# Optimization experiments

Measured on AMD Instinct MI355X. Metric: run time of the kernel, lower is better.

Reference implementation:

```python
import jax, jax.numpy as jnp
import numpy as np


def conv2d(x, w, b, pad):
    out = jax.lax.conv_general_dilated(x, w, (1, 1), ((pad, pad), (pad, pad)),
                                       dimension_numbers=('NCHW', 'OIHW', 'NCHW'))
    return out + b[None, :, None, None]


def silu(x):
    return x * jax.nn.sigmoid(x)


def group_norm(x, g, b, groups, eps=1e-5):
    B, C, H, W = x.shape
    xg = x.reshape(B, groups, C // groups, H, W)
    m = xg.mean(axis=(2, 3, 4), keepdims=True)
    v = xg.var(axis=(2, 3, 4), keepdims=True)
    xg = (xg - m) * jax.lax.rsqrt(v + eps)
    return xg.reshape(B, C, H, W) * g[None, :, None, None] + b[None, :, None, None]


def snake_cumsum(off):
    # off: [B,K,H,W]. Center kernel point has zero offset; points accumulate
    # outward from center (the 'snake' bend), as in DSCNet.
    K = off.shape[1]
    c = K // 2
    upper = jnp.cumsum(off[:, c + 1:], axis=1)
    lower = jnp.flip(jnp.cumsum(jnp.flip(off[:, :c], axis=1), axis=1), axis=1)
    return jnp.concatenate([lower, jnp.zeros_like(off[:, :1]), upper], axis=1)


def bilinear_gather(img, ys, xs):
    # img [B,C,H,W]; ys,xs [B,K,H,W] float coords -> sampled [B,C,K,H,W]
    B, C, H, W = img.shape
    K = ys.shape[1]
    ys = jnp.clip(ys, 0.0, H - 1.0)
    xs = jnp.clip(xs, 0.0, W - 1.0)
    y0f = jnp.floor(ys)
    x0f = jnp.floor(xs)
    wy = (ys - y0f)[:, None]  # [B,1,K,H,W]
    wx = (xs - x0f)[:, None]
    y0 = y0f.astype(jnp.int32)
    x0 = x0f.astype(jnp.int32)
    y1 = jnp.minimum(y0 + 1, H - 1)
    x1 = jnp.minimum(x0 + 1, W - 1)
    flat = img.reshape(B, C, H * W)

    def gat(yi, xi):
        idx = (yi * W + xi).reshape(B, -1)  # [B, K*H*W]
        g = jnp.take_along_axis(flat, idx[:, None, :], axis=2)
        return g.reshape(B, C, K, H, W)

    return (gat(y0, x0) * (1 - wy) * (1 - wx) + gat(y0, x1) * (1 - wy) * wx
            + gat(y1, x0) * wy * (1 - wx) + gat(y1, x1) * wy * wx)


def dsconv(x, off_w, off_b, dsc_w, dsc_b, gn_g, gn_b, morph, extend_scope=1.0):
    # Dynamic snake conv for one morphology.
    # morph 0: kernel spreads along x, bends in y; morph 1: opposite.
    B, C, H, W = x.shape
    K = dsc_w.shape[-1]
    c = K // 2
    off = jnp.tanh(conv2d(x, off_w, off_b, pad=1))  # [B,2K,H,W]; BN folded into conv bias
    bend = snake_cumsum(off[:, :K] if morph == 0 else off[:, K:])  # [B,K,H,W]
    spread = (jnp.arange(K) - c).astype(x.dtype)[None, :, None, None]
    hh = jnp.arange(H, dtype=x.dtype)[None, None, :, None]
    ww = jnp.arange(W, dtype=x.dtype)[None, None, None, :]
    if morph == 0:
        ys = hh + extend_scope * bend
        xs = jnp.broadcast_to(ww + spread, ys.shape)
    else:
        xs = ww + extend_scope * bend
        ys = jnp.broadcast_to(hh + spread, xs.shape)
    sampled = bilinear_gather(x, ys, xs)  # [B,C,K,H,W]
    # k-point conv over the stacked snake axis == (K,1)/(1,K) conv with stride K
    out = jnp.einsum('bckhw,ock->bohw', sampled, dsc_w) + dsc_b[None, :, None, None]
    O = dsc_w.shape[0]
    return jax.nn.relu(group_norm(out, gn_g, gn_b, groups=O // 4))


def dysnake_conv(x, p):
    # DySnakeConv: standard conv + snake-x + snake-y, concat, 1x1 fuse
    kpad = p['conv0_w'].shape[-1] // 2
    a = silu(conv2d(x, p['conv0_w'], p['conv0_b'], pad=kpad))
    bx = dsconv(x, p['offx_w'], p['offx_b'], p['dscx_w'], p['dscx_b'], p['gnx_g'], p['gnx_b'], morph=0)
    by = dsconv(x, p['offy_w'], p['offy_b'], p['dscy_w'], p['dscy_b'], p['gny_g'], p['gny_b'], morph=1)
    cat = jnp.concatenate([a, bx, by], axis=1)  # [B,3*ouc,H,W]
    return silu(jnp.einsum('bchw,oc->bohw', cat, p['fuse_w']) + p['fuse_b'][None, :, None, None])


_PNAMES = ['conv0_w', 'conv0_b', 'offx_w', 'offx_b', 'dscx_w', 'dscx_b', 'gnx_g', 'gnx_b',
           'offy_w', 'offy_b', 'dscy_w', 'dscy_b', 'gny_g', 'gny_b', 'fuse_w', 'fuse_b']


def setup_inputs() -> dict:
    key = jax.random.key(0)
    ks = iter(jax.random.split(key, 64))

    def rn(shape, s=0.05):
        return jax.random.normal(next(ks), shape, dtype=jnp.float32) * s

    B, H, W = 8, 80, 80
    c1, c2, c_ = 256, 256, 128
    kk = 3

    def block(inc, ouc, pre):
        return {
            pre + 'conv0_w': rn((ouc, inc, kk, kk)), pre + 'conv0_b': rn((ouc,)),
            pre + 'offx_w': rn((2 * kk, inc, 3, 3)), pre + 'offx_b': rn((2 * kk,)),
            pre + 'dscx_w': rn((ouc, inc, kk)), pre + 'dscx_b': rn((ouc,)),
            pre + 'gnx_g': jnp.ones((ouc,), jnp.float32), pre + 'gnx_b': jnp.zeros((ouc,), jnp.float32),
            pre + 'offy_w': rn((2 * kk, inc, 3, 3)), pre + 'offy_b': rn((2 * kk,)),
            pre + 'dscy_w': rn((ouc, inc, kk)), pre + 'dscy_b': rn((ouc,)),
            pre + 'gny_g': jnp.ones((ouc,), jnp.float32), pre + 'gny_b': jnp.zeros((ouc,), jnp.float32),
            pre + 'fuse_w': rn((ouc, 3 * ouc)), pre + 'fuse_b': rn((ouc,)),
        }

    inp = {'x': jax.random.normal(next(ks), (B, c1, H, W), dtype=jnp.float32)}
    inp.update(block(c1, c_, 'cv1_'))
    inp.update(block(c_, c2, 'cv2_'))
    return inp


def reference(x, cv1_conv0_w, cv1_conv0_b, cv1_offx_w, cv1_offx_b, cv1_dscx_w, cv1_dscx_b,
              cv1_gnx_g, cv1_gnx_b, cv1_offy_w, cv1_offy_b, cv1_dscy_w, cv1_dscy_b,
              cv1_gny_g, cv1_gny_b, cv1_fuse_w, cv1_fuse_b,
              cv2_conv0_w, cv2_conv0_b, cv2_offx_w, cv2_offx_b, cv2_dscx_w, cv2_dscx_b,
              cv2_gnx_g, cv2_gnx_b, cv2_offy_w, cv2_offy_b, cv2_dscy_w, cv2_dscy_b,
              cv2_gny_g, cv2_gny_b, cv2_fuse_w, cv2_fuse_b):
    p1 = dict(zip(_PNAMES, (cv1_conv0_w, cv1_conv0_b, cv1_offx_w, cv1_offx_b, cv1_dscx_w, cv1_dscx_b,
                            cv1_gnx_g, cv1_gnx_b, cv1_offy_w, cv1_offy_b, cv1_dscy_w, cv1_dscy_b,
                            cv1_gny_g, cv1_gny_b, cv1_fuse_w, cv1_fuse_b)))
    p2 = dict(zip(_PNAMES, (cv2_conv0_w, cv2_conv0_b, cv2_offx_w, cv2_offx_b, cv2_dscx_w, cv2_dscx_b,
                            cv2_gnx_g, cv2_gnx_b, cv2_offy_w, cv2_offy_b, cv2_dscy_w, cv2_dscy_b,
                            cv2_gny_g, cv2_gny_b, cv2_fuse_w, cv2_fuse_b)))
    h = dysnake_conv(x, p1)
    h = dysnake_conv(h, p2)
    return x + h  # shortcut and c1 == c2
```

## Files before the change

### kernel.cpp

```cpp
#include <hip/hip_runtime.h>
#include <cstddef>

#define B_   8
#define H_   80
#define W_   80
#define HW   6400
#define W2   82
#define HW2  6724

typedef __attribute__((ext_vector_type(8)))  short short8;
typedef __attribute__((ext_vector_type(16))) float f32x16;

__device__ __forceinline__ float bf2f(ushort u) {
    return __uint_as_float(((unsigned)u) << 16);
}
__device__ __forceinline__ ushort f2bf(float f) {
    unsigned u = __float_as_uint(f);
    u += 0x7FFF + ((u >> 16) & 1);
    return (ushort)(u >> 16);
}
__device__ __forceinline__ f32x16 mfma16(short8 a, short8 b, f32x16 c) {
    return __builtin_amdgcn_mfma_f32_32x32x16_bf16(a, b, c, 0, 0, 0);
}
__device__ __forceinline__ void async16(const void* g, void* l) {
    __builtin_amdgcn_global_load_lds(
        (const __attribute__((address_space(1))) unsigned int*)g,
        (__attribute__((address_space(3))) unsigned int*)l, 16, 0, 0);
}
__device__ __forceinline__ const ushort* frag_ptr(const ushort* sbuf, int row, int c8l) {
    return sbuf + row * 64 + ((c8l ^ (row & 7)) << 3);
}

__global__ __launch_bounds__(256) void halo_zero2_kernel(
    ushort* __restrict__ xp1, ushort* __restrict__ xp2) {
    int idx = blockIdx.x * 256 + threadIdx.x;
    const int n1 = B_ * 324 * 32;
    const int n2 = B_ * 324 * 16;
    ushort* xp; int C, slots, i;
    if (idx < n1) { xp = xp1; C = 256; slots = 32; i = idx; }
    else if (idx < n1 + n2) { xp = xp2; C = 128; slots = 16; i = idx - n1; }
    else return;
    int sl = i % slots;
    int t = i / slots;
    int p = t % 324;
    int b = t / 324;
    int h, w;
    if (p < 164) { h = (p < 82) ? 0 : 81; w = p % 82; }
    else { int q = p - 164; w = (q < 80) ? 0 : 81; h = 1 + (q % 80); }
    *(uint4*)(xp + ((size_t)(b * HW2 + h * W2 + w)) * C + sl * 8) =
        make_uint4(0, 0, 0, 0);
}

__global__ __launch_bounds__(256) void transpose_x_kernel(
    const float* __restrict__ x, ushort* __restrict__ xp, int C) {
    __shared__ float s[64][65];
    int hw0 = blockIdx.x * 64, c0 = blockIdx.y * 64, b = blockIdx.z;
    int t = threadIdx.x;
    int hl = t & 63, cq = t >> 6;
    #pragma unroll
    for (int i = 0; i < 16; i++) {
        int cl = cq * 16 + i;
        s[cl][hl] = x[((size_t)(b * C + c0 + cl)) * HW + hw0 + hl];
    }
    __syncthreads();
    int cl = t & 63, hq = t >> 6;
    #pragma unroll
    for (int i = 0; i < 16; i++) {
        int hl2 = hq * 16 + i;
        int hw = hw0 + hl2;
        int h = hw / W_, w = hw - h * W_;
        xp[((size_t)(b * HW2 + (h + 1) * W2 + w + 1)) * C + c0 + cl] = f2bf(s[cl][hl2]);
    }
}

__global__ __launch_bounds__(256) void final_add_kernel(
    const float* __restrict__ x, const ushort* __restrict__ h2,
    float* __restrict__ out, int C) {
    __shared__ float s[64][65];
    int hw0 = blockIdx.x * 64, c0 = blockIdx.y * 64, b = blockIdx.z;
    int t = threadIdx.x;
    int cl = t & 63, hq = t >> 6;
    #pragma unroll
    for (int i = 0; i < 16; i++) {
        int hl = hq * 16 + i;
        s[cl][hl] = bf2f(h2[((size_t)(b * HW + hw0 + hl)) * C + c0 + cl]);
    }
    __syncthreads();
    int hl = t & 63, cq = t >> 6;
    #pragma unroll
    for (int i = 0; i < 16; i++) {
        int cl2 = cq * 16 + i;
        size_t o = ((size_t)(b * C + c0 + cl2)) * HW + hw0 + hl;
        out[o] = x[o] + s[cl2][hl];
    }
}

struct WJobs {
    const float* src[8];
    ushort* dst[8];
    int cin[8], t[8];
    int start[9];
};

__global__ __launch_bounds__(256) void wprep_all_kernel(WJobs J) {
    int idx = blockIdx.x * 256 + threadIdx.x;
    if (idx >= J.start[8]) return;
    int j = 0;
    #pragma unroll
    for (int k = 1; k < 8; k++) if (idx >= J.start[k]) j = k;
    int i = idx - J.start[j];
    int CIN = J.cin[j], T = J.t[j];
    int oc = i / (CIN * T);
    int r = i - oc * CIN * T;
    int ci = r / T, t_ = r - ci * T;
    J.dst[j][((size_t)oc * T + t_) * CIN + ci] = f2bf(J.src[j][i]);
}

__global__ void wprep_off_kernel(const float* __restrict__ wx_,
                                 const float* __restrict__ bx_,
                                 const float* __restrict__ wy_,
                                 const float* __restrict__ by_,
                                 ushort* __restrict__ dst,
                                 float* __restrict__ bdst, int CIN) {
    int idx = blockIdx.x * 256 + threadIdx.x;
    if (idx < 4) {
        const int chs[4] = {0, 2, 3, 5};
        bdst[idx] = (idx < 2) ? bx_[chs[idx]] : by_[chs[idx]];
    }
    if (idx >= 32 * 9 * CIN) return;
    int oc = idx / (9 * CIN);
    int r = idx - oc * 9 * CIN;
    int tap = r / CIN, ci = r - tap * CIN;
    float v = 0.f;
    if (oc < 4) {
        const int chs[4] = {0, 2, 3, 5};
        const float* src = (oc < 2) ? wx_ : wy_;
        v = src[((size_t)chs[oc] * CIN + ci) * 9 + tap];
    }
    dst[idx] = f2bf(v);
}

__global__ __launch_bounds__(256, 2) void off_conv_mfma_kernel(
    const ushort* __restrict__ xp, const ushort* __restrict__ wB,
    const float* __restrict__ bias, float* __restrict__ off4, int CIN) {
    __shared__ ushort s_x[162 * 64];
    __shared__ ushort s_w[144 * 64];
    int tid = threadIdx.x;
    int ty0 = (blockIdx.x / 5) * 16, tx0 = (blockIdx.x % 5) * 16;
    int b = blockIdx.y;
    int lane = tid & 63, wid = tid >> 6;
    int l31 = lane & 31, kg = lane >> 5;
    int pym[2], pxm[2];
    #pragma unroll
    for (int mf = 0; mf < 2; mf++) {
        int p = wid * 64 + mf * 32 + l31;
        pym[mf] = p >> 4; pxm[mf] = p & 15;
    }
    f32x16 acc[2] = {};
    for (int c0 = 0; c0 < CIN; c0 += 32) {
        __syncthreads();
        for (int u = tid; u < 1296; u += 256) {
            int pid = u >> 2, ci8 = u & 3;
            int r = pid / 18, c = pid - r * 18;
            int py = ty0 + r, px = tx0 + c;
            uint4 v = *(const uint4*)(xp + ((size_t)(b * HW2 + py * W2 + px)) * CIN
                                      + c0 + ci8 * 8);
            int row = pid >> 1;
            int phys = (((pid & 1) << 2) + ci8) ^ (row & 7);
            *(uint4*)(s_x + row * 64 + phys * 8) = v;
        }
        for (int cc = wid; cc < 18; cc += 4) {
            int L = cc * 64 + lane;
            int row = L >> 3, phys = L & 7;
            int logical = phys ^ (row & 7);
            int tap = row >> 4, ocp = row & 15;
            int oc = ocp * 2 + (logical >> 2), ci8 = logical & 3;
            async16(wB + ((size_t)oc * 9 + tap) * CIN + c0 + ci8 * 8,
                    s_w + (size_t)L * 8);
        }
        __syncthreads();
        #pragma unroll
        for (int tap = 0; tap < 9; tap++) {
            int dy = tap / 3, dx = tap - dy * 3;
            int wrow = tap * 16 + (l31 >> 1);
            #pragma unroll
            for (int ks = 0; ks < 2; ks++) {
                int blk = ks * 2 + kg;
                int wphys = (((l31 & 1) << 2) + blk) ^ (wrow & 7);
                short8 bfr = *(const short8*)(s_w + wrow * 64 + wphys * 8);
                #pragma unroll
                for (int mf = 0; mf < 2; mf++) {
                    int pix = (pym[mf] + dy) * 18 + (pxm[mf] + dx);
                    int xrow = pix >> 1;
                    int xphys = (((pix & 1) << 2) + blk) ^ (xrow & 7);
                    short8 afr = *(const short8*)(s_x + xrow * 64 + xphys * 8);
                    acc[mf] = mfma16(afr, bfr, acc[mf]);
                }
            }
        }
    }
    int oc = l31;
    if (oc < 4) {
        float bb = bias[oc];
        #pragma unroll
        for (int mf = 0; mf < 2; mf++) {
            #pragma unroll
            for (int reg = 0; reg < 16; reg++) {
                int row = (reg & 3) + 8 * (reg >> 2) + 4 * kg;
                int p = wid * 64 + mf * 32 + row;
                int y = ty0 + (p >> 4), x = tx0 + (p & 15);
                off4[((size_t)b * 4 + oc) * HW + y * W_ + x] = tanhf(acc[mf][reg] + bb);
            }
        }
    }
}

__global__ __launch_bounds__(256, 4) void convdsc_kernel(
    const ushort* __restrict__ xp,
    const ushort* __restrict__ wC, const float* __restrict__ biasC,
    ushort* __restrict__ outC,
    const float* __restrict__ off4,
    const ushort* __restrict__ Bwx, const float* __restrict__ biasx,
    ushort* __restrict__ outx,
    const ushort* __restrict__ Bwy, const float* __restrict__ biasy,
    ushort* __restrict__ outy, float* __restrict__ stat, int CIN, int OC) {
    __shared__ ushort s_a[128 * 64];
    __shared__ ushort s_b[128 * 64];
    __shared__ int   s_i0[3][128];
    __shared__ int   s_i1[3][128];
    __shared__ float s_wl[3][128];
    int tid = threadIdx.x;
    int m0 = blockIdx.x * 128, n0 = blockIdx.y * 128;
    int b = m0 / HW, hw0 = m0 - b * HW;
    int lane = tid & 63, wid = tid >> 6;
    int l31 = lane & 31, kg = lane >> 5;
    int wm = wid >> 1, wn = wid & 1;

    if (blockIdx.z == 0) {
        const ushort* xpb = xp + (size_t)b * HW2 * CIN;
        const ushort* asrc[4];
        #pragma unroll
        for (int j = 0; j < 4; j++) {
            int s = (wid * 4 + j) * 64 + lane;
            int r = s >> 3, c8p = s & 7;
            int c8l = c8p ^ (r & 7);
            int hw = hw0 + r;
            int h = hw / W_, w = hw - h * W_;
            asrc[j] = xpb + ((size_t)((h + 1) * W2 + (w + 1))) * CIN + c8l * 8;
        }
        f32x16 acc[2][2] = {};
        int K = 9 * CIN, nk = K >> 6;
        int tap = 0, cioff = 0;
        for (int kc = 0; kc < nk; kc++) {
            int kg64 = kc << 6;
            int dy = tap / 3, dx = tap - dy * 3;
            int soff = ((dy - 1) * W2 + (dx - 1)) * CIN + cioff;
            __syncthreads();
            #pragma unroll
            for (int j = 0; j < 4; j++) {
                int s = (wid * 4 + j) * 64 + lane;
                int r = s >> 3, c8p = s & 7;
                int c8l = c8p ^ (r & 7);
                async16(wC + (size_t)(n0 + r) * K + kg64 + c8l * 8, s_b + s * 8);
                async16(asrc[j] + soff, s_a + s * 8);
            }
            __syncthreads();
            #pragma unroll
            for (int ks = 0; ks < 4; ks++) {
                int c8l = ks * 2 + kg;
                short8 af0 = *(const short8*)frag_ptr(s_a, wm * 64 + l31, c8l);
                short8 af1 = *(const short8*)frag_ptr(s_a, wm * 64 + 32 + l31, c8l);
                short8 bf0 = *(const short8*)frag_ptr(s_b, wn * 64 + l31, c8l);
                short8 bf1 = *(const short8*)frag_ptr(s_b, wn * 64 + 32 + l31, c8l);
                acc[0][0] = mfma16(af0, bf0, acc[0][0]);
                acc[0][1] = mfma16(af0, bf1, acc[0][1]);
                acc[1][0] = mfma16(af1, bf0, acc[1][0]);
                acc[1][1] = mfma16(af1, bf1, acc[1][1]);
            }
            cioff += 64;
            if (cioff == CIN) { cioff = 0; tap++; }
        }
        #pragma unroll
        for (int nf = 0; nf < 2; nf++) {
            int n = n0 + wn * 64 + nf * 32 + l31;
            float bb = biasC[n];
            #pragma unroll
            for (int mf = 0; mf < 2; mf++) {
                #pragma unroll
                for (int reg = 0; reg < 16; reg++) {
                    int row = (reg & 3) + 8 * (reg >> 2) + 4 * kg;
                    int m = m0 + wm * 64 + mf * 32 + row;
                    float v = acc[mf][nf][reg] + bb;
                    v = v / (1.f + expf(-v));
                    outC[(size_t)m * OC + n] = f2bf(v);
                }
            }
        }
        return;
    }

    int morph = blockIdx.z - 1;
    const ushort* Bw = morph ? Bwy : Bwx;
    const float* bias = morph ? biasy : biasx;
    ushort* out = morph ? outy : outx;
    float* statm = stat + (size_t)morph * B_ * 256 * 2;
    for (int u = tid; u < 384; u += 256) {
        int k3 = u >> 7, r = u & 127;
        int hw = hw0 + r;
        int h = hw / W_, w = hw - h * W_;
        float bend = 0.f;
        if (k3 != 1) {
            int mp = (morph ? 2 : 0) + (k3 >> 1);
            bend = off4[((size_t)b * 4 + mp) * HW + hw];
        }
        int i0, i1; float wl;
        if (morph == 0) {
            float ys = fminf(fmaxf((float)h + bend, 0.f), 79.f);
            float y0f = floorf(ys); wl = ys - y0f;
            int y0 = (int)y0f, y1 = min(y0 + 1, 79);
            int xk = min(max(w + k3 - 1, 0), 79);
            i0 = (y0 + 1) * W2 + xk + 1; i1 = (y1 + 1) * W2 + xk + 1;
        } else {
            float xs = fminf(fmaxf((float)w + bend, 0.f), 79.f);
            float x0f = floorf(xs); wl = xs - x0f;
            int x0 = (int)x0f, x1 = min(x0 + 1, 79);
            int yk = min(max(h + k3 - 1, 0), 79);
            i0 = (yk + 1) * W2 + x0 + 1; i1 = (yk + 1) * W2 + x1 + 1;
        }
        s_i0[k3][r] = i0; s_i1[k3][r] = i1; s_wl[k3][r] = wl;
    }
    const ushort* xb = xp + (size_t)b * HW2 * CIN;
    const ushort* asrcC[4];
    #pragma unroll
    for (int j = 0; j < 4; j++) {
        int s = (wid * 4 + j) * 64 + lane;
        int r = s >> 3, c8p = s & 7;
        int c8l = c8p ^ (r & 7);
        int hw = hw0 + r;
        int h = hw / W_, w = hw - h * W_;
        asrcC[j] = xb + ((size_t)((h + 1) * W2 + (w + 1))) * CIN + c8l * 8;
    }
    f32x16 acc[2][2] = {};
    int K = 3 * CIN, nk = K >> 6;
    for (int kc = 0; kc < nk; kc++) {
        int kg64 = kc << 6;
        int k3 = kg64 / CIN;
        int cioff = kg64 - k3 * CIN;
        __syncthreads();
        #pragma unroll
        for (int j = 0; j < 4; j++) {
            int s = (wid * 4 + j) * 64 + lane;
            int r = s >> 3, c8p = s & 7;
            int c8l = c8p ^ (r & 7);
            async16(Bw + (size_t)(n0 + r) * K + kg64 + c8l * 8, s_b + s * 8);
        }
        if (k3 == 1) {
            #pragma unroll
            for (int j = 0; j < 4; j++) {
                int s = (wid * 4 + j) * 64 + lane;
                async16(asrcC[j] + cioff, s_a + s * 8);
            }
        } else {
            #pragma unroll
            for (int i = 0; i < 4; i++) {
                int s = i * 256 + tid;
                int r = s >> 3, c8p = s & 7;
                int c8l = c8p ^ (r & 7);
                int ci = cioff + c8l * 8;
                float wl = s_wl[k3][r];
                uint4 u0 = *(const uint4*)(xb + (size_t)s_i0[k3][r] * CIN + ci);
                uint4 u1 = *(const uint4*)(xb + (size_t)s_i1[k3][r] * CIN + ci);
                const ushort* p0 = (const ushort*)&u0;
                const ushort* p1 = (const ushort*)&u1;
                uint ov[4];
                #pragma unroll
                for (int j = 0; j < 4; j++) {
                    float a0 = bf2f(p0[2 * j]),     b0 = bf2f(p1[2 * j]);
                    float a1 = bf2f(p0[2 * j + 1]), b1 = bf2f(p1[2 * j + 1]);
                    float r0 = a0 + (b0 - a0) * wl;
                    float r1 = a1 + (b1 - a1) * wl;
                    asm("v_cvt_pk_bf16_f32 %0, %1, %2"
                        : "=v"(ov[j]) : "v"(r0), "v"(r1));
                }
                *(uint4*)(s_a + s * 8) = *(uint4*)ov;
            }
        }
        __syncthreads();
        #pragma unroll
        for (int ks = 0; ks < 4; ks++) {
            int c8l = ks * 2 + kg;
            short8 af0 = *(const short8*)frag_ptr(s_a, wm * 64 + l31, c8l);
            short8 af1 = *(const short8*)frag_ptr(s_a, wm * 64 + 32 + l31, c8l);
            short8 bf0 = *(const short8*)frag_ptr(s_b, wn * 64 + l31, c8l);
            short8 bf1 = *(const short8*)frag_ptr(s_b, wn * 64 + 32 + l31, c8l);
            acc[0][0] = mfma16(af0, bf0, acc[0][0]);
            acc[0][1] = mfma16(af0, bf1, acc[0][1]);
            acc[1][0] = mfma16(af1, bf0, acc[1][0]);
            acc[1][1] = mfma16(af1, bf1, acc[1][1]);
        }
    }
    #pragma unroll
    for (int nf = 0; nf < 2; nf++) {
        int n = n0 + wn * 64 + nf * 32 + l31;
        float bb = bias[n];
        float ssum = 0.f, ssq = 0.f;
        #pragma unroll
        for (int mf = 0; mf < 2; mf++) {
            #pragma unroll
            for (int reg = 0; reg < 16; reg++) {
                int row = (reg & 3) + 8 * (reg >> 2) + 4 * kg;
                int m = m0 + wm * 64 + mf * 32 + row;
                float v = acc[mf][nf][reg] + bb;
                ssum += v; ssq += v * v;
                out[(size_t)m * OC + n] = f2bf(v);
            }
        }
        ssum += __shfl_xor(ssum, 32);
        ssq  += __shfl_xor(ssq, 32);
        if (kg == 0) {
            float* st = statm + ((size_t)b * OC + n) * 2;
            atomicAdd(st, ssum);
            atomicAdd(st + 1, ssq);
        }
    }
}

__global__ __launch_bounds__(256, 4) void gemm128_kernel(
    const ushort* __restrict__ a0, const ushort* __restrict__ a1,
    const ushort* __restrict__ a2, int part_k,
    const ushort* __restrict__ Bw, int K, int N,
    const float* __restrict__ bias,
    const float* __restrict__ scx, const float* __restrict__ shx,
    const float* __restrict__ scy, const float* __restrict__ shy,
    ushort* __restrict__ out, int epi_silu, int out_pad) {
    __shared__ ushort s_a[128 * 64];
    __shared__ ushort s_b[128 * 64];
    int tid = threadIdx.x;
    int m0 = blockIdx.x * 128, n0 = blockIdx.y * 128;
    int b = m0 / HW;
    int lane = tid & 63, wid = tid >> 6;
    int l31 = lane & 31, kg = lane >> 5;
    int wm = wid >> 1, wn = wid & 1;
    f32x16 acc[2][2] = {};
    int nk = K >> 6;
    for (int kc = 0; kc < nk; kc++) {
        int kg64 = kc << 6;
        int part = kg64 / part_k;
        int koff = kg64 - part * part_k;
        __syncthreads();
        #pragma unroll
        for (int j = 0; j < 4; j++) {
            int s = (wid * 4 + j) * 64 + lane;
            int r = s >> 3, c8p = s & 7;
            int c8l = c8p ^ (r & 7);
            async16(Bw + (size_t)(n0 + r) * K + kg64 + c8l * 8, s_b + s * 8);
        }
        if (part == 0) {
            #pragma unroll
            for (int j = 0; j < 4; j++) {
                int s = (wid * 4 + j) * 64 + lane;
                int r = s >> 3, c8p = s & 7;
                int c8l = c8p ^ (r & 7);
                async16(a0 + (size_t)(m0 + r) * part_k + koff + c8l * 8,
                        s_a + s * 8);
            }
        } else {
            const ushort* ap = (part == 1) ? a1 : a2;
            const float* scp = ((part == 1) ? scx : scy) + (size_t)b * part_k;
            const float* shp = ((part == 1) ? shx : shy) + (size_t)b * part_k;
            #pragma unroll
            for (int i = 0; i < 4; i++) {
                int s = i * 256 + tid;
                int r = s >> 3, c8p = s & 7;
                int c8l = c8p ^ (r & 7);
                int ch = koff + c8l * 8;
                uint4 u = *(const uint4*)(ap + (size_t)(m0 + r) * part_k + ch);
                float4 c0 = *(const float4*)(scp + ch);
                float4 c1 = *(const float4*)(scp + ch + 4);
                float4 h0 = *(const float4*)(shp + ch);
                float4 h1 = *(const float4*)(shp + ch + 4);
                const ushort* pv = (const ushort*)&u;
                uint ov[4];
                float r0, r1;
                r0 = fmaxf(bf2f(pv[0]) * c0.x + h0.x, 0.f);
                r1 = fmaxf(bf2f(pv[1]) * c0.y + h0.y, 0.f);
                asm("v_cvt_pk_bf16_f32 %0, %1, %2" : "=v"(ov[0]) : "v"(r0), "v"(r1));
                r0 = fmaxf(bf2f(pv[2]) * c0.z + h0.z, 0.f);
                r1 = fmaxf(bf2f(pv[3]) * c0.w + h0.w, 0.f);
                asm("v_cvt_pk_bf16_f32 %0, %1, %2" : "=v"(ov[1]) : "v"(r0), "v"(r1));
                r0 = fmaxf(bf2f(pv[4]) * c1.x + h1.x, 0.f);
                r1 = fmaxf(bf2f(pv[5]) * c1.y + h1.y, 0.f);
                asm("v_cvt_pk_bf16_f32 %0, %1, %2" : "=v"(ov[2]) : "v"(r0), "v"(r1));
                r0 = fmaxf(bf2f(pv[6]) * c1.z + h1.z, 0.f);
                r1 = fmaxf(bf2f(pv[7]) * c1.w + h1.w, 0.f);
                asm("v_cvt_pk_bf16_f32 %0, %1, %2" : "=v"(ov[3]) : "v"(r0), "v"(r1));
                *(uint4*)(s_a + s * 8) = *(uint4*)ov;
            }
        }
        __syncthreads();
        #pragma unroll
        for (int ks = 0; ks < 4; ks++) {
            int c8l = ks * 2 + kg;
            short8 af0 = *(const short8*)frag_ptr(s_a, wm * 64 + l31, c8l);
            short8 af1 = *(const short8*)frag_ptr(s_a, wm * 64 + 32 + l31, c8l);
            short8 bf0 = *(const short8*)frag_ptr(s_b, wn * 64 + l31, c8l);
            short8 bf1 = *(const short8*)frag_ptr(s_b, wn * 64 + 32 + l31, c8l);
            acc[0][0] = mfma16(af0, bf0, acc[0][0]);
            acc[0][1] = mfma16(af0, bf1, acc[0][1]);
            acc[1][0] = mfma16(af1, bf0, acc[1][0]);
            acc[1][1] = mfma16(af1, bf1, acc[1][1]);
        }
    }
    #pragma unroll
    for (int nf = 0; nf < 2; nf++) {
        int n = n0 + wn * 64 + nf * 32 + l31;
        float bb = bias[n];
        #pragma unroll
        for (int mf = 0; mf < 2; mf++) {
            #pragma unroll
            for (int reg = 0; reg < 16; reg++) {
                int row = (reg & 3) + 8 * (reg >> 2) + 4 * kg;
                int m = m0 + wm * 64 + mf * 32 + row;
                float v = acc[mf][nf][reg] + bb;
                if (epi_silu) v = v / (1.f + expf(-v));
                size_t mm = (size_t)m;
                if (out_pad) {
                    int bb_ = m / HW, hw = m - bb_ * HW;
                    int h = hw / W_, w = hw - h * W_;
                    mm = (size_t)bb_ * HW2 + (h + 1) * W2 + w + 1;
                }
                out[mm * N + n] = f2bf(v);
            }
        }
    }
}

__global__ void gn_finalize_kernel(const float* __restrict__ stat,
                                   const float* __restrict__ gx,
                                   const float* __restrict__ bx,
                                   const float* __restrict__ gy,
                                   const float* __restrict__ by,
                                   float* __restrict__ scx, float* __restrict__ shx,
                                   float* __restrict__ scy, float* __restrict__ shy,
                                   int C) {
    int idx = blockIdx.x * 256 + threadIdx.x;
    if (idx >= B_ * C) return;
    int which = blockIdx.y;
    const float* gamma = which ? gy : gx;
    const float* beta  = which ? by : bx;
    float* sc = which ? scy : scx;
    float* sh = which ? shy : shx;
    int b = idx / C, c = idx - b * C;
    const float* st = stat + (size_t)which * B_ * 256 * 2
                    + ((size_t)b * C + (c & ~3)) * 2;
    float s  = st[0] + st[2] + st[4] + st[6];
    float sq = st[1] + st[3] + st[5] + st[7];
    float mean = s / (4.f * HW);
    float var = sq / (4.f * HW) - mean * mean;
    float rs = rsqrtf(var + 1e-5f);
    float scale = rs * gamma[c];
    sc[idx] = scale;
    sh[idx] = beta[c] - mean * scale;
}

struct BlkBuf {
    ushort *xp, *abuf, *bqx, *bqy, *hout;
    float *off4, *stat, *scx, *shx, *scy, *shy, *boff;
    ushort *wc, *wdx, *wdy, *wf, *woff;
};

static void run_block(const BlkBuf& B, int CIN, int OC,
                      const float* const* P, int out_pad, hipStream_t stream) {
    dim3 blk(256);
    hipMemsetAsync(B.stat, 0, (size_t)2 * B_ * 256 * 2 * 4, stream);
    off_conv_mfma_kernel<<<dim3(25, B_), blk, 0, stream>>>(
        B.xp, B.woff, B.boff, B.off4, CIN);
    convdsc_kernel<<<dim3(400, OC / 128, 3), blk, 0, stream>>>(
        B.xp, B.wc, P[1], B.abuf,
        B.off4, B.wdx, P[5], B.bqx, B.wdy, P[11], B.bqy, B.stat, CIN, OC);
    int fgrid = (B_ * OC + 255) / 256;
    gn_finalize_kernel<<<dim3(fgrid, 2), blk, 0, stream>>>(
        B.stat, P[6], P[7], P[12], P[13], B.scx, B.shx, B.scy, B.shy, OC);
    gemm128_kernel<<<dim3(400, OC / 128), blk, 0, stream>>>(
        B.abuf, B.bqx, B.bqy, OC, B.wf, 3 * OC, OC, P[15],
        B.scx, B.shx, B.scy, B.shy, B.hout, 1, out_pad);
}

extern "C" void kernel_launch(void* const* d_in, const int* in_sizes, int n_in,
                              void* d_out, int out_size, void* d_ws, size_t ws_size,
                              hipStream_t stream) {
    const float* x = (const float*)d_in[0];
    const float* P1[16];
    const float* P2[16];
    for (int i = 0; i < 16; i++) {
        P1[i] = (const float*)d_in[1 + i];
        P2[i] = (const float*)d_in[17 + i];
    }
    char* base = (char*)d_ws;
    size_t off = 0;
    auto alloc = [&](size_t bytes) -> char* {
        off = (off + 255) & ~(size_t)255;
        char* p = base + off;
        off += bytes;
        return p;
    };
    ushort* xp1  = (ushort*)alloc((size_t)B_ * HW2 * 256 * 2);
    ushort* xp2  = (ushort*)alloc((size_t)B_ * HW2 * 128 * 2);
    ushort* abuf = (ushort*)alloc((size_t)B_ * HW * 256 * 2);
    ushort* bqx  = (ushort*)alloc((size_t)B_ * HW * 256 * 2);
    ushort* bqy  = (ushort*)alloc((size_t)B_ * HW * 256 * 2);
    float*  off4 = (float*)alloc((size_t)B_ * 4 * HW * 4);
    float*  stat = (float*)alloc((size_t)2 * B_ * 256 * 2 * 4);
    float*  scx  = (float*)alloc(B_ * 256 * 4);
    float*  shx  = (float*)alloc(B_ * 256 * 4);
    float*  scy  = (float*)alloc(B_ * 256 * 4);
    float*  shy  = (float*)alloc(B_ * 256 * 4);
    ushort* wc1  = (ushort*)alloc((size_t)128 * 9 * 256 * 2);
    ushort* wc2  = (ushort*)alloc((size_t)256 * 9 * 128 * 2);
    ushort* wdx1 = (ushort*)alloc((size_t)128 * 3 * 256 * 2);
    ushort* wdy1 = (ushort*)alloc((size_t)128 * 3 * 256 * 2);
    ushort* wdx2 = (ushort*)alloc((size_t)256 * 3 * 128 * 2);
    ushort* wdy2 = (ushort*)alloc((size_t)256 * 3 * 128 * 2);
    ushort* wf1  = (ushort*)alloc((size_t)128 * 384 * 2);
    ushort* wf2  = (ushort*)alloc((size_t)256 * 768 * 2);
    ushort* wo1  = (ushort*)alloc((size_t)32 * 9 * 256 * 2);
    ushort* wo2  = (ushort*)alloc((size_t)32 * 9 * 128 * 2);
    float*  bo1  = (float*)alloc(32 * 4);
    float*  bo2  = (float*)alloc(32 * 4);
    ushort* h2 = xp1;

    dim3 blk(256);
    {
        int total = B_ * 324 * 32 + B_ * 324 * 16;
        halo_zero2_kernel<<<(total + 255) / 256, blk, 0, stream>>>(xp1, xp2);
    }

    {
        WJobs J;
        const float* srcs[8] = {P1[0], P1[4], P1[10], P1[14],
                                P2[0], P2[4], P2[10], P2[14]};
        ushort* dsts[8] = {wc1, wdx1, wdy1, wf1, wc2, wdx2, wdy2, wf2};
        int cins[8] = {256, 256, 256, 384, 128, 128, 128, 768};
        int ts[8]   = {9, 3, 3, 1, 9, 3, 3, 1};
        int ocs[8]  = {128, 128, 128, 128, 256, 256, 256, 256};
        int acc = 0;
        for (int j = 0; j < 8; j++) {
            J.src[j] = srcs[j]; J.dst[j] = dsts[j];
            J.cin[j] = cins[j]; J.t[j] = ts[j];
            J.start[j] = acc;
            acc += ocs[j] * cins[j] * ts[j];
        }
        J.start[8] = acc;
        wprep_all_kernel<<<(acc + 255) / 256, blk, 0, stream>>>(J);
    }
    wprep_off_kernel<<<(32 * 9 * 256 + 255) / 256, blk, 0, stream>>>(
        P1[2], P1[3], P1[8], P1[9], wo1, bo1, 256);
    wprep_off_kernel<<<(32 * 9 * 128 + 255) / 256, blk, 0, stream>>>(
        P2[2], P2[3], P2[8], P2[9], wo2, bo2, 128);

    transpose_x_kernel<<<dim3(100, 4, B_), blk, 0, stream>>>(x, xp1, 256);

    BlkBuf B1 = {xp1, abuf, bqx, bqy, xp2, off4, stat, scx, shx, scy, shy,
                 bo1, wc1, wdx1, wdy1, wf1, wo1};
    run_block(B1, 256, 128, P1, 1, stream);

    BlkBuf B2 = {xp2, abuf, bqx, bqy, h2, off4, stat, scx, shx, scy, shy,
                 bo2, wc2, wdx2, wdy2, wf2, wo2};
    run_block(B2, 128, 256, P2, 0, stream);

    final_add_kernel<<<dim3(100, 4, B_), blk, 0, stream>>>(x, h2, (float*)d_out, 256);
}
```

Before: 524.7 us.

## Recast offset conv as implicit GEMM with more blocks; restructure GEMM epilogues

The offset convolution kernel moves from 16x16 spatial tiles with a halo (200 blocks, 32-channel chunks) to an implicit-GEMM layout. Each block now takes 128 pixels and walks K in 64-wide chunks using async loads, giving 400 blocks at higher occupancy. The goal is to fill the GPU better for this small-N conv, at the price of losing the halo reuse, so input rows are reloaded once per tap. The epilogues of the three GEMM kernels are also reordered to handle both N fragments in one loop, with the bias loads hoisted and the paired stores interleaved.

```diff
diff --git a/kernel.cpp b/kernel.cpp
--- a/kernel.cpp
+++ b/kernel.cpp
@@ -140,77 +140,63 @@
     dst[idx] = f2bf(v);
 }
 
-__global__ __launch_bounds__(256, 2) void off_conv_mfma_kernel(
+__global__ __launch_bounds__(256, 4) void off_gemm_kernel(
     const ushort* __restrict__ xp, const ushort* __restrict__ wB,
     const float* __restrict__ bias, float* __restrict__ off4, int CIN) {
-    __shared__ ushort s_x[162 * 64];
-    __shared__ ushort s_w[144 * 64];
+    __shared__ ushort s_a[128 * 64];
+    __shared__ ushort s_bo[32 * 64];
     int tid = threadIdx.x;
-    int ty0 = (blockIdx.x / 5) * 16, tx0 = (blockIdx.x % 5) * 16;
-    int b = blockIdx.y;
+    int m0 = blockIdx.x * 128;
+    int b = m0 / HW, hw0 = m0 - b * HW;
     int lane = tid & 63, wid = tid >> 6;
     int l31 = lane & 31, kg = lane >> 5;
-    int pym[2], pxm[2];
-    #pragma unroll
-    for (int mf = 0; mf < 2; mf++) {
-        int p = wid * 64 + mf * 32 + l31;
-        pym[mf] = p >> 4; pxm[mf] = p & 15;
-    }
-    f32x16 acc[2] = {};
-    for (int c0 = 0; c0 < CIN; c0 += 32) {
+    const ushort* xpb = xp + (size_t)b * HW2 * CIN;
+    const ushort* asrc[4];
+    #pragma unroll
+    for (int j = 0; j < 4; j++) {
+        int s = (wid * 4 + j) * 64 + lane;
+        int r = s >> 3, c8p = s & 7;
+        int c8l = c8p ^ (r & 7);
+        int hw = hw0 + r;
+        int h = hw / W_, w = hw - h * W_;
+        asrc[j] = xpb + ((size_t)((h + 1) * W2 + (w + 1))) * CIN + c8l * 8;
+    }
+    int rB = tid >> 3;
+    int cB = (tid & 7) ^ (rB & 7);
+    f32x16 acc = {};
+    int K = 9 * CIN, nk = K >> 6;
+    int tap = 0, cioff = 0;
+    for (int kc = 0; kc < nk; kc++) {
+        int kg64 = kc << 6;
+        int dy = tap / 3, dx = tap - dy * 3;
+        int soff = ((dy - 1) * W2 + (dx - 1)) * CIN + cioff;
         __syncthreads();
-        for (int u = tid; u < 1296; u += 256) {
-            int pid = u >> 2, ci8 = u & 3;
-            int r = pid / 18, c = pid - r * 18;
-            int py = ty0 + r, px = tx0 + c;
-            uint4 v = *(const uint4*)(xp + ((size_t)(b * HW2 + py * W2 + px)) * CIN
-                                      + c0 + ci8 * 8);
-            int row = pid >> 1;
-            int phys = (((pid & 1) << 2) + ci8) ^ (row & 7);
-            *(uint4*)(s_x + row * 64 + phys * 8) = v;
-        }
-        for (int cc = wid; cc < 18; cc += 4) {
-            int L = cc * 64 + lane;
-            int row = L >> 3, phys = L & 7;
-            int logical = phys ^ (row & 7);
-            int tap = row >> 4, ocp = row & 15;
-            int oc = ocp * 2 + (logical >> 2), ci8 = logical & 3;
-            async16(wB + ((size_t)oc * 9 + tap) * CIN + c0 + ci8 * 8,
-                    s_w + (size_t)L * 8);
+        async16(wB + (size_t)rB * K + kg64 + cB * 8, s_bo + (size_t)tid * 8);
+        #pragma unroll
+        for (int j = 0; j < 4; j++) {
+            int s = (wid * 4 + j) * 64 + lane;
+            async16(asrc[j] + soff, s_a + s * 8);
         }
         __syncthreads();
         #pragma unroll
-        for (int tap = 0; tap < 9; tap++) {
-            int dy = tap / 3, dx = tap - dy * 3;
-            int wrow = tap * 16 + (l31 >> 1);
-            #pragma unroll
-            for (int ks = 0; ks < 2; ks++) {
-                int blk = ks * 2 + kg;
-                int wphys = (((l31 & 1) << 2) + blk) ^ (wrow & 7);
-                short8 bfr = *(const short8*)(s_w + wrow * 64 + wphys * 8);
-                #pragma unroll
-                for (int mf = 0; mf < 2; mf++) {
-                    int pix = (pym[mf] + dy) * 18 + (pxm[mf] + dx);
-                    int xrow = pix >> 1;
-                    int xphys = (((pix & 1) << 2) + blk) ^ (xrow & 7);
-                    short8 afr = *(const short8*)(s_x + xrow * 64 + xphys * 8);
-                    acc[mf] = mfma16(afr, bfr, acc[mf]);
-                }
-            }
-        }
+        for (int ks = 0; ks < 4; ks++) {
+            int c8l = ks * 2 + kg;
+            short8 af = *(const short8*)frag_ptr(s_a, wid * 32 + l31, c8l);
+            short8 bf = *(const short8*)frag_ptr(s_bo, l31, c8l);
+            acc = mfma16(af, bf, acc);
+        }
+        cioff += 64;
+        if (cioff == CIN) { cioff = 0; tap++; }
     }
     int oc = l31;
     if (oc < 4) {
         float bb = bias[oc];
         #pragma unroll
-        for (int mf = 0; mf < 2; mf++) {
-            #pragma unroll
-            for (int reg = 0; reg < 16; reg++) {
-                int row = (reg & 3) + 8 * (reg >> 2) + 4 * kg;
-                int p = wid * 64 + mf * 32 + row;
-                int y = ty0 + (p >> 4), x = tx0 + (p & 15);
-                off4[((size_t)b * 4 + oc) * HW + y * W_ + x] = tanhf(acc[mf][reg] + bb);
-            }
+        for (int reg = 0; reg < 16; reg++) {
+            int row = (reg & 3) + 8 * (reg >> 2) + 4 * kg;
+            int m = m0 + wid * 32 + row;
+            int hw = m - b * HW;
+            off4[((size_t)b * 4 + oc) * HW + hw] = tanhf(acc[reg] + bb);
         }
     }
 }
@@ -280,20 +266,20 @@
             cioff += 64;
             if (cioff == CIN) { cioff = 0; tap++; }
         }
-        #pragma unroll
-        for (int nf = 0; nf < 2; nf++) {
-            int n = n0 + wn * 64 + nf * 32 + l31;
-            float bb = biasC[n];
+        int na = n0 + wn * 64 + l31, nb = na + 32;
+        float ba = biasC[na], bb2 = biasC[nb];
+        #pragma unroll
+        for (int mf = 0; mf < 2; mf++) {
             #pragma unroll
-            for (int mf = 0; mf < 2; mf++) {
-                #pragma unroll
-                for (int reg = 0; reg < 16; reg++) {
-                    int row = (reg & 3) + 8 * (reg >> 2) + 4 * kg;
-                    int m = m0 + wm * 64 + mf * 32 + row;
-                    float v = acc[mf][nf][reg] + bb;
-                    v = v / (1.f + expf(-v));
-                    outC[(size_t)m * OC + n] = f2bf(v);
-                }
+            for (int reg = 0; reg < 16; reg++) {
+                int row = (reg & 3) + 8 * (reg >> 2) + 4 * kg;
+                int m = m0 + wm * 64 + mf * 32 + row;
+                float v0 = acc[mf][0][reg] + ba;
+                float v1 = acc[mf][1][reg] + bb2;
+                v0 = v0 / (1.f + expf(-v0));
+                v1 = v1 / (1.f + expf(-v1));
+                outC[(size_t)m * OC + na] = f2bf(v0);
+                outC[(size_t)m * OC + nb] = f2bf(v1);
             }
         }
         return;
@@ -399,29 +385,34 @@
             acc[1][1] = mfma16(af1, bf1, acc[1][1]);
         }
     }
-    #pragma unroll
-    for (int nf = 0; nf < 2; nf++) {
-        int n = n0 + wn * 64 + nf * 32 + l31;
-        float bb = bias[n];
-        float ssum = 0.f, ssq = 0.f;
-        #pragma unroll
-        for (int mf = 0; mf < 2; mf++) {
-            #pragma unroll
-            for (int reg = 0; reg < 16; reg++) {
-                int row = (reg & 3) + 8 * (reg >> 2) + 4 * kg;
-                int m = m0 + wm * 64 + mf * 32 + row;
-                float v = acc[mf][nf][reg] + bb;
-                ssum += v; ssq += v * v;
-                out[(size_t)m * OC + n] = f2bf(v);
-            }
-        }
-        ssum += __shfl_xor(ssum, 32);
-        ssq  += __shfl_xor(ssq, 32);
-        if (kg == 0) {
-            float* st = statm + ((size_t)b * OC + n) * 2;
-            atomicAdd(st, ssum);
-            atomicAdd(st + 1, ssq);
-        }
+    int na = n0 + wn * 64 + l31, nb = na + 32;
+    float ba = bias[na], bb2 = bias[nb];
+    float ssum0 = 0.f, ssq0 = 0.f, ssum1 = 0.f, ssq1 = 0.f;
+    #pragma unroll
+    for (int mf = 0; mf < 2; mf++) {
+        #pragma unroll
+        for (int reg = 0; reg < 16; reg++) {
+            int row = (reg & 3) + 8 * (reg >> 2) + 4 * kg;
+            int m = m0 + wm * 64 + mf * 32 + row;
+            float v0 = acc[mf][0][reg] + ba;
+            float v1 = acc[mf][1][reg] + bb2;
+            ssum0 += v0; ssq0 += v0 * v0;
+            ssum1 += v1; ssq1 += v1 * v1;
+            out[(size_t)m * OC + na] = f2bf(v0);
+            out[(size_t)m * OC + nb] = f2bf(v1);
+        }
+    }
+    ssum0 += __shfl_xor(ssum0, 32);
+    ssq0  += __shfl_xor(ssq0, 32);
+    ssum1 += __shfl_xor(ssum1, 32);
+    ssq1  += __shfl_xor(ssq1, 32);
+    if (kg == 0) {
+        float* st0 = statm + ((size_t)b * OC + na) * 2;
+        atomicAdd(st0, ssum0);
+        atomicAdd(st0 + 1, ssq0);
+        float* st1 = statm + ((size_t)b * OC + nb) * 2;
+        atomicAdd(st1, ssum1);
+        atomicAdd(st1 + 1, ssq1);
     }
 }
 
@@ -511,26 +502,28 @@
             acc[1][1] = mfma16(af1, bf1, acc[1][1]);
         }
     }
-    #pragma unroll
-    for (int nf = 0; nf < 2; nf++) {
-        int n = n0 + wn * 64 + nf * 32 + l31;
-        float bb = bias[n];
-        #pragma unroll
-        for (int mf = 0; mf < 2; mf++) {
-            #pragma unroll
-            for (int reg = 0; reg < 16; reg++) {
-                int row = (reg & 3) + 8 * (reg >> 2) + 4 * kg;
-                int m = m0 + wm * 64 + mf * 32 + row;
-                float v = acc[mf][nf][reg] + bb;
-                if (epi_silu) v = v / (1.f + expf(-v));
-                size_t mm = (size_t)m;
-                if (out_pad) {
-                    int bb_ = m / HW, hw = m - bb_ * HW;
-                    int h = hw / W_, w = hw - h * W_;
-                    mm = (size_t)bb_ * HW2 + (h + 1) * W2 + w + 1;
-                }
-                out[mm * N + n] = f2bf(v);
-            }
+    int na = n0 + wn * 64 + l31, nb = na + 32;
+    float ba = bias[na], bb2 = bias[nb];
+    #pragma unroll
+    for (int mf = 0; mf < 2; mf++) {
+        #pragma unroll
+        for (int reg = 0; reg < 16; reg++) {
+            int row = (reg & 3) + 8 * (reg >> 2) + 4 * kg;
+            int m = m0 + wm * 64 + mf * 32 + row;
+            float v0 = acc[mf][0][reg] + ba;
+            float v1 = acc[mf][1][reg] + bb2;
+            if (epi_silu) {
+                v0 = v0 / (1.f + expf(-v0));
+                v1 = v1 / (1.f + expf(-v1));
+            }
+            size_t mm = (size_t)m;
+            if (out_pad) {
+                int bb_ = m / HW, hw = m - bb_ * HW;
+                int h = hw / W_, w = hw - h * W_;
+                mm = (size_t)bb_ * HW2 + (h + 1) * W2 + w + 1;
+            }
+            out[mm * N + na] = f2bf(v0);
+            out[mm * N + nb] = f2bf(v1);
         }
     }
 }
@@ -573,7 +566,7 @@
                       const float* const* P, int out_pad, hipStream_t stream) {
     dim3 blk(256);
     hipMemsetAsync(B.stat, 0, (size_t)2 * B_ * 256 * 2 * 4, stream);
-    off_conv_mfma_kernel<<<dim3(25, B_), blk, 0, stream>>>(
+    off_gemm_kernel<<<dim3(B_ * HW / 128), blk, 0, stream>>>(
         B.xp, B.woff, B.boff, B.off4, CIN);
     convdsc_kernel<<<dim3(400, OC / 128, 3), blk, 0, stream>>>(
         B.xp, B.wc, P[1], B.abuf,
```

New measurement: 491.3 us. 1.07x faster.
